# Kernel optimization log

Hardware: AMD Instinct MI355X
Metric: run time of the kernel (lower is better)

## Reference

```python
import jax, jax.numpy as jnp
import numpy as np

ALPHA = 0.25
GAMMA = 2.0
HUBER_DELTA = 0.5  # init kwarg delta
REG_BETA = 1.0 / 9.0


def calc_iou(a, b):
    # a: [A,4] anchors, b: [M,4] gt boxes, xyxy
    area = (b[:, 2] - b[:, 0]) * (b[:, 3] - b[:, 1])  # [M]
    iw = jnp.clip(jnp.minimum(a[:, 2:3], b[:, 2]) - jnp.maximum(a[:, 0:1], b[:, 0]), 0.0)
    ih = jnp.clip(jnp.minimum(a[:, 3:4], b[:, 3]) - jnp.maximum(a[:, 1:2], b[:, 1]), 0.0)
    ua = jnp.clip(((a[:, 2] - a[:, 0]) * (a[:, 3] - a[:, 1]))[:, None] + area - iw * ih, 1e-8)
    return iw * ih / ua  # [A,M]


def _per_sample(cls, reg, dist, ann, anchor):
    # cls [A,C], reg [A,4], dist [A,1], ann [M,6], anchor [A,4]
    aw = anchor[:, 2] - anchor[:, 0]
    ah = anchor[:, 3] - anchor[:, 1]
    acx = anchor[:, 0] + 0.5 * aw
    acy = anchor[:, 1] + 0.5 * ah

    valid = ann[:, 4] != -1.0  # padding annotations have class == -1
    cls = jnp.clip(cls, 1e-4, 1.0 - 1e-4)

    iou = jnp.where(valid[None, :], calc_iou(anchor, ann[:, :4]), -1.0)  # [A,M]
    iou_max = iou.max(axis=1)
    iou_arg = iou.argmax(axis=1)
    assigned = ann[iou_arg]  # [A,6]

    pos = iou_max >= 0.5
    num_pos = pos.sum()
    denom = jnp.maximum(num_pos.astype(cls.dtype), 1.0)

    labels = assigned[:, 4].astype(jnp.int32)
    onehot = jax.nn.one_hot(labels, cls.shape[1], dtype=cls.dtype)
    # -1 = ignore, 0 = negative (IoU<0.4 or positive-but-not-this-class), 1 = assigned class
    targets = jnp.where(pos[:, None], onehot,
                        jnp.where((iou_max < 0.4)[:, None], 0.0, -1.0))

    af = jnp.where(targets == 1.0, ALPHA, 1.0 - ALPHA)
    fw = af * jnp.where(targets == 1.0, 1.0 - cls, cls) ** GAMMA
    bce = -(targets * jnp.log(cls) + (1.0 - targets) * jnp.log(1.0 - cls))
    cls_loss = jnp.where(targets != -1.0, fw * bce, 0.0).sum() / denom

    # empty-annotation fallback: all anchors treated as background
    cls_loss_empty = ((1.0 - ALPHA) * cls ** GAMMA * (-jnp.log(1.0 - cls))).sum()
    has_ann = valid.any()
    cls_loss = jnp.where(has_ann, cls_loss, cls_loss_empty)

    gw_raw = assigned[:, 2] - assigned[:, 0]
    gh_raw = assigned[:, 3] - assigned[:, 1]
    gcx = assigned[:, 0] + 0.5 * gw_raw  # centers use unclamped w/h (as in torch code)
    gcy = assigned[:, 1] + 0.5 * gh_raw
    gw = jnp.clip(gw_raw, 1.0)
    gh = jnp.clip(gh_raw, 1.0)
    t = jnp.stack([(gcx - acx) / aw, (gcy - acy) / ah,
                   jnp.log(gw / aw), jnp.log(gh / ah)], axis=1)
    t = t / jnp.asarray([0.1, 0.1, 0.2, 0.2], dtype=cls.dtype)
    diff = jnp.abs(t - reg)
    rl = jnp.where(diff <= REG_BETA, 0.5 * 9.0 * diff ** 2, diff - 0.5 / 9.0)
    posf = pos.astype(cls.dtype)
    reg_loss = jnp.where(num_pos > 0, (rl * posf[:, None]).sum() / (denom * 4.0), 0.0)

    # --- distance Huber loss (delta=0.5), positives only ---
    d = jnp.abs(dist[:, 0] - assigned[:, 5])
    hl = jnp.where(d <= HUBER_DELTA, 0.5 * d ** 2, HUBER_DELTA * (d - 0.5 * HUBER_DELTA))
    dist_loss = jnp.where(num_pos > 0, (hl * posf).sum() / denom, 0.0)

    return cls_loss, reg_loss, dist_loss


def reference(classifications, regressions, distances, anchors, annotations):
    anchor = anchors[0]
    cl, rl, dl = jax.vmap(_per_sample, in_axes=(0, 0, 0, 0, None))(
        classifications, regressions, distances, annotations, anchor)
    return (jnp.mean(cl, keepdims=True),
            jnp.mean(rl, keepdims=True),
            jnp.mean(dl, keepdims=True))


def setup_inputs() -> dict:
    key = jax.random.key(0)
    ks = jax.random.split(key, 10)
    B, A, C, M = 8, 120000, 80, 32
    IMG = 800.0

    classifications = jax.random.uniform(ks[0], (B, A, C), dtype=jnp.float32)
    regressions = jax.random.normal(ks[1], (B, A, 4), dtype=jnp.float32)
    distances = jax.random.normal(ks[2], (B, A, 1), dtype=jnp.float32) * 10.0 + 50.0

    # anchors: valid xyxy boxes over an 800px image
    acx = jax.random.uniform(ks[3], (A,), minval=0.0, maxval=IMG)
    acy = jax.random.uniform(ks[4], (A,), minval=0.0, maxval=IMG)
    aw = jax.random.uniform(ks[5], (A, 2), minval=16.0, maxval=256.0)
    anchors = jnp.stack([acx - 0.5 * aw[:, 0], acy - 0.5 * aw[:, 1],
                         acx + 0.5 * aw[:, 0], acy + 0.5 * aw[:, 1]], axis=1)[None].astype(jnp.float32)

    # annotations: [B,M,6] = x1,y1,x2,y2,class,distance (all valid)
    gc = jax.random.uniform(ks[6], (B, M, 2), minval=100.0, maxval=IMG - 100.0)
    gs = jax.random.uniform(ks[7], (B, M, 2), minval=32.0, maxval=300.0)
    boxes = jnp.concatenate([gc - 0.5 * gs, gc + 0.5 * gs], axis=-1)
    labels = jax.random.randint(ks[8], (B, M, 1), 0, C).astype(jnp.float32)
    gdist = jax.random.uniform(ks[9], (B, M, 1), minval=1.0, maxval=100.0)
    annotations = jnp.concatenate([boxes, labels, gdist], axis=-1).astype(jnp.float32)

    return {"classifications": classifications, "regressions": regressions,
            "distances": distances, "anchors": anchors, "annotations": annotations}
```

## Files before the change

kernel.cpp:

```cpp
#include <hip/hip_runtime.h>
#include <hip/hip_bf16.h>


__device__ __forceinline__ float wave_reduce_sum(float v) {
#pragma unroll
    for (int off = 32; off > 0; off >>= 1) v += __shfl_down(v, off);
    return v;
}

__device__ __forceinline__ float smooth_l1(float d) {
    return d <= (1.0f / 9.0f) ? 4.5f * d * d : d - (0.5f / 9.0f);
}

template <int CPA>
__global__ __launch_bounds__(256) void fused_kernel(
    const float* __restrict__ cls, const float* __restrict__ reg,
    const float* __restrict__ dist, const float* __restrict__ anchors,
    const float* __restrict__ ann, float4* __restrict__ partials,
    int A, int M, int nb) {
    const int b = blockIdx.y;
    const int base = blockIdx.x << 8;
    const int tid = threadIdx.x;

    __shared__ float s_ann[64 * 6];
    __shared__ signed char s_state[256];
    const float* annb = ann + (size_t)b * M * 6;
    for (int i = tid; i < M * 6; i += 256) s_ann[i] = annb[i];
    s_state[tid] = -2;
    __syncthreads();

    const int a = base + tid;
    float l_npos = 0.f, l_reg = 0.f, l_dist = 0.f;
    if (a < A) {
        const float4 av = *(const float4*)(anchors + (size_t)a * 4);
        const float aw = av.z - av.x, ah = av.w - av.y;
        const float acx = av.x + 0.5f * aw, acy = av.y + 0.5f * ah;
        const float aarea = aw * ah;

        float best = -1.0f;
        int bi = 0;
        for (int m = 0; m < M; ++m) {
            const float* g = s_ann + m * 6;
            float iou = -1.0f;
            if (g[4] != -1.0f) {
                float iw = fmaxf(fminf(av.z, g[2]) - fmaxf(av.x, g[0]), 0.f);
                float ih = fmaxf(fminf(av.w, g[3]) - fmaxf(av.y, g[1]), 0.f);
                float inter = iw * ih;
                float area = (g[2] - g[0]) * (g[3] - g[1]);
                float ua = fmaxf(aarea + area - inter, 1e-8f);
                iou = inter / ua;
            }
            if (iou > best) { best = iou; bi = m; }
        }

        signed char st;
        if (best >= 0.5f) {
            const float* g = s_ann + bi * 6;
            st = (signed char)(int)g[4];
            l_npos = 1.f;
            const float4 rv = *(const float4*)(reg + ((size_t)b * A + a) * 4);
            const float gwr = g[2] - g[0], ghr = g[3] - g[1];
            const float gcx = g[0] + 0.5f * gwr, gcy = g[1] + 0.5f * ghr;
            const float gw = fmaxf(gwr, 1.f), gh = fmaxf(ghr, 1.f);
            const float t0 = ((gcx - acx) / aw) / 0.1f;
            const float t1 = ((gcy - acy) / ah) / 0.1f;
            const float t2 = __logf(gw / aw) / 0.2f;
            const float t3 = __logf(gh / ah) / 0.2f;
            l_reg = smooth_l1(fabsf(t0 - rv.x)) + smooth_l1(fabsf(t1 - rv.y)) +
                    smooth_l1(fabsf(t2 - rv.z)) + smooth_l1(fabsf(t3 - rv.w));
            const float dv = dist[(size_t)b * A + a];
            const float dd = fabsf(dv - g[5]);
            l_dist = dd <= 0.5f ? 0.5f * dd * dd : 0.5f * (dd - 0.25f);
        } else if (best < 0.4f) {
            st = -1;
        } else {
            st = -2;
        }
        s_state[tid] = st;
    }
    __syncthreads();

    const float4* __restrict__ clsb =
        (const float4*)(cls + ((size_t)b * A + base) * (CPA * 4));
    int a_local = tid / CPA;
    int cc = tid % CPA;
    constexpr int dA = 256 / CPA;
    constexpr int dC = 256 % CPA;
    float lsum = 0.f;
#pragma unroll 4
    for (int k = 0; k < CPA; ++k) {
        const int st = s_state[a_local];
        if (st != -2) {
            const float4 cv = clsb[k * 256 + tid];
            const int c0 = cc << 2;
#pragma unroll
            for (int j = 0; j < 4; ++j) {
                float c = j == 0 ? cv.x : j == 1 ? cv.y : j == 2 ? cv.z : cv.w;
                c = fminf(fmaxf(c, 1e-4f), 1.0f - 1e-4f);
                const bool ispos = (st == c0 + j);
                const float om = 1.0f - c;
                const float x = ispos ? c : om;
                const float w = ispos ? 0.25f * om * om : 0.75f * c * c;
                lsum -= w * __logf(x);
            }
        }
        a_local += dA;
        cc += dC;
        if (cc >= CPA) { cc -= CPA; ++a_local; }
    }

    __shared__ float s_red[4][4];
    const float w0 = wave_reduce_sum(l_npos);
    const float w1 = wave_reduce_sum(lsum);
    const float w2 = wave_reduce_sum(l_reg);
    const float w3 = wave_reduce_sum(l_dist);
    const int lane = tid & 63, wid = tid >> 6;
    if (lane == 0) {
        s_red[0][wid] = w0; s_red[1][wid] = w1; s_red[2][wid] = w2; s_red[3][wid] = w3;
    }
    __syncthreads();
    if (tid == 0) {
        float4 p;
        p.x = s_red[0][0] + s_red[0][1] + s_red[0][2] + s_red[0][3];
        p.y = s_red[1][0] + s_red[1][1] + s_red[1][2] + s_red[1][3];
        p.z = s_red[2][0] + s_red[2][1] + s_red[2][2] + s_red[2][3];
        p.w = s_red[3][0] + s_red[3][1] + s_red[3][2] + s_red[3][3];
        partials[(size_t)b * nb + blockIdx.x] = p;
    }
}

__global__ void finalize_kernel(const float4* __restrict__ partials,
                                float* __restrict__ out, int B, int nb) {
    const int lane = threadIdx.x & 63;
    const int b = threadIdx.x >> 6;
    __shared__ float s_res[8][3];
    if (b < B) {
        float np_ = 0.f, cs = 0.f, rs = 0.f, ds = 0.f;
        for (int i = lane; i < nb; i += 64) {
            const float4 p = partials[(size_t)b * nb + i];
            np_ += p.x; cs += p.y; rs += p.z; ds += p.w;
        }
        np_ = wave_reduce_sum(np_);
        cs = wave_reduce_sum(cs);
        rs = wave_reduce_sum(rs);
        ds = wave_reduce_sum(ds);
        if (lane == 0) {
            const float denom = fmaxf(np_, 1.f);
            s_res[b][0] = cs / denom;
            s_res[b][1] = np_ > 0.f ? rs / (denom * 4.f) : 0.f;
            s_res[b][2] = np_ > 0.f ? ds / denom : 0.f;
        }
    }
    __syncthreads();
    if (threadIdx.x == 0) {
        float c = 0.f, r = 0.f, d = 0.f;
        for (int i = 0; i < B; ++i) { c += s_res[i][0]; r += s_res[i][1]; d += s_res[i][2]; }
        out[0] = c / (float)B;
        out[1] = r / (float)B;
        out[2] = d / (float)B;
    }
}

__global__ __launch_bounds__(256) void fused_generic_kernel(
    const float* __restrict__ cls, const float* __restrict__ reg,
    const float* __restrict__ dist, const float* __restrict__ anchors,
    const float* __restrict__ ann, float4* __restrict__ partials,
    int A, int C, int M, int nb) {
    const int b = blockIdx.y;
    const int base = blockIdx.x << 8;
    const int tid = threadIdx.x;
    const int cpa = C >> 2;

    __shared__ float s_ann[64 * 6];
    __shared__ signed char s_state[256];
    const float* annb = ann + (size_t)b * M * 6;
    for (int i = tid; i < M * 6; i += 256) s_ann[i] = annb[i];
    s_state[tid] = -2;
    __syncthreads();

    const int a = base + tid;
    float l_npos = 0.f, l_reg = 0.f, l_dist = 0.f;
    if (a < A) {
        const float4 av = *(const float4*)(anchors + (size_t)a * 4);
        const float aw = av.z - av.x, ah = av.w - av.y;
        const float acx = av.x + 0.5f * aw, acy = av.y + 0.5f * ah;
        const float aarea = aw * ah;
        float best = -1.0f;
        int bi = 0;
        for (int m = 0; m < M; ++m) {
            const float* g = s_ann + m * 6;
            float iou = -1.0f;
            if (g[4] != -1.0f) {
                float iw = fmaxf(fminf(av.z, g[2]) - fmaxf(av.x, g[0]), 0.f);
                float ih = fmaxf(fminf(av.w, g[3]) - fmaxf(av.y, g[1]), 0.f);
                float inter = iw * ih;
                float area = (g[2] - g[0]) * (g[3] - g[1]);
                float ua = fmaxf(aarea + area - inter, 1e-8f);
                iou = inter / ua;
            }
            if (iou > best) { best = iou; bi = m; }
        }
        signed char st;
        if (best >= 0.5f) {
            const float* g = s_ann + bi * 6;
            st = (signed char)(int)g[4];
            l_npos = 1.f;
            const float4 rv = *(const float4*)(reg + ((size_t)b * A + a) * 4);
            const float gwr = g[2] - g[0], ghr = g[3] - g[1];
            const float gcx = g[0] + 0.5f * gwr, gcy = g[1] + 0.5f * ghr;
            const float gw = fmaxf(gwr, 1.f), gh = fmaxf(ghr, 1.f);
            const float t0 = ((gcx - acx) / aw) / 0.1f;
            const float t1 = ((gcy - acy) / ah) / 0.1f;
            const float t2 = __logf(gw / aw) / 0.2f;
            const float t3 = __logf(gh / ah) / 0.2f;
            l_reg = smooth_l1(fabsf(t0 - rv.x)) + smooth_l1(fabsf(t1 - rv.y)) +
                    smooth_l1(fabsf(t2 - rv.z)) + smooth_l1(fabsf(t3 - rv.w));
            const float dv = dist[(size_t)b * A + a];
            const float dd = fabsf(dv - g[5]);
            l_dist = dd <= 0.5f ? 0.5f * dd * dd : 0.5f * (dd - 0.25f);
        } else if (best < 0.4f) {
            st = -1;
        } else {
            st = -2;
        }
        s_state[tid] = st;
    }
    __syncthreads();

    const float4* __restrict__ clsb = (const float4*)(cls + ((size_t)b * A + base) * C);
    int a_local = tid / cpa;
    int cc = tid % cpa;
    const int dA = 256 / cpa;
    const int dC = 256 % cpa;
    float lsum = 0.f;
    for (int k = 0; k < cpa; ++k) {
        const int st = s_state[a_local];
        if (st != -2) {
            const float4 cv = clsb[k * 256 + tid];
            const int c0 = cc << 2;
#pragma unroll
            for (int j = 0; j < 4; ++j) {
                float c = j == 0 ? cv.x : j == 1 ? cv.y : j == 2 ? cv.z : cv.w;
                c = fminf(fmaxf(c, 1e-4f), 1.0f - 1e-4f);
                const bool ispos = (st == c0 + j);
                const float om = 1.0f - c;
                const float x = ispos ? c : om;
                const float w = ispos ? 0.25f * om * om : 0.75f * c * c;
                lsum -= w * __logf(x);
            }
        }
        a_local += dA;
        cc += dC;
        if (cc >= cpa) { cc -= cpa; ++a_local; }
    }

    __shared__ float s_red[4][4];
    const float w0 = wave_reduce_sum(l_npos);
    const float w1 = wave_reduce_sum(lsum);
    const float w2 = wave_reduce_sum(l_reg);
    const float w3 = wave_reduce_sum(l_dist);
    const int lane = tid & 63, wid = tid >> 6;
    if (lane == 0) {
        s_red[0][wid] = w0; s_red[1][wid] = w1; s_red[2][wid] = w2; s_red[3][wid] = w3;
    }
    __syncthreads();
    if (tid == 0) {
        float4 p;
        p.x = s_red[0][0] + s_red[0][1] + s_red[0][2] + s_red[0][3];
        p.y = s_red[1][0] + s_red[1][1] + s_red[1][2] + s_red[1][3];
        p.z = s_red[2][0] + s_red[2][1] + s_red[2][2] + s_red[2][3];
        p.w = s_red[3][0] + s_red[3][1] + s_red[3][2] + s_red[3][3];
        partials[(size_t)b * nb + blockIdx.x] = p;
    }
}

extern "C" void kernel_launch(void* const* d_in, const int* in_sizes, int n_in,
                              void* d_out, int out_size, void* d_ws, size_t ws_size,
                              hipStream_t stream) {
    const float* cls     = (const float*)d_in[0];
    const float* reg     = (const float*)d_in[1];
    const float* dist    = (const float*)d_in[2];
    const float* anchors = (const float*)d_in[3];
    const float* ann     = (const float*)d_in[4];

    const int A = in_sizes[3] / 4;
    const int B = in_sizes[1] / (A * 4);
    const int C = in_sizes[0] / (B * A);
    const int M = in_sizes[4] / (B * 6);
    const int nb = (A + 255) / 256;

    float4* partials = (float4*)d_ws;

    dim3 g(nb, B), blk(256);
    if (C == 80) {
        fused_kernel<20><<<g, blk, 0, stream>>>(cls, reg, dist, anchors, ann,
                                                partials, A, M, nb);
    } else {
        fused_generic_kernel<<<g, blk, 0, stream>>>(cls, reg, dist, anchors, ann,
                                                    partials, A, C, M, nb);
    }
    finalize_kernel<<<1, B * 64, 0, stream>>>(partials, (float*)d_out, B, nb);
}
```

Baseline: 92.20 us.

## Compute background focal loss unconditionally and apply sparse per-anchor corrections

The classification loop now sums the negative focal term for every class of every anchor without first waiting on the IoU assignment, using nontemporal loads issued before the IoU loop. Ignored anchors and the positive class entry are then corrected sparsely: a wave ballot walks the non-background anchors, subtracting the full row for ignored anchors and swapping in the positive term for the assigned class. This removes the shared-memory state array and the barrier between assignment and the streaming loop, so the bulk class loads can overlap the IoU work. In exchange it adds serial per-anchor wave loops whose cost grows with the number of positive and ignored anchors, and it changes floating-point summation order.

```diff
diff --git a/kernel.cpp b/kernel.cpp
--- a/kernel.cpp
+++ b/kernel.cpp
@@ -1,6 +1,10 @@
 #include <hip/hip_runtime.h>
 #include <hip/hip_bf16.h>
 
+
+typedef float v4f __attribute__((ext_vector_type(4)));
+
+#define LN2_075 0.51986038542f
 
 __device__ __forceinline__ float wave_reduce_sum(float v) {
 #pragma unroll
@@ -21,16 +25,44 @@
     const int b = blockIdx.y;
     const int base = blockIdx.x << 8;
     const int tid = threadIdx.x;
+    const int lane = tid & 63;
 
     __shared__ float s_ann[64 * 6];
-    __shared__ signed char s_state[256];
     const float* annb = ann + (size_t)b * M * 6;
     for (int i = tid; i < M * 6; i += 256) s_ann[i] = annb[i];
-    s_state[tid] = -2;
+
+    const v4f* __restrict__ clsb = (const v4f*)(cls + ((size_t)b * A + base) * (CPA * 4));
+    float acc2 = 0.f;
+    if (base + 256 <= A) {
+#pragma unroll
+        for (int k = 0; k < CPA; ++k) {
+            const v4f cv = __builtin_nontemporal_load(&clsb[k * 256 + tid]);
+#pragma unroll
+            for (int j = 0; j < 4; ++j) {
+                const float c = fminf(fmaxf(cv[j], 1e-4f), 1.0f - 1e-4f);
+                acc2 = fmaf(c * c, __log2f(1.0f - c), acc2);
+            }
+        }
+    } else {
+        const int nch = (A - base) * CPA;
+        for (int k = 0; k < CPA; ++k) {
+            const int idx = k * 256 + tid;
+            if (idx < nch) {
+                const v4f cv = __builtin_nontemporal_load(&clsb[idx]);
+#pragma unroll
+                for (int j = 0; j < 4; ++j) {
+                    const float c = fminf(fmaxf(cv[j], 1e-4f), 1.0f - 1e-4f);
+                    acc2 = fmaf(c * c, __log2f(1.0f - c), acc2);
+                }
+            }
+        }
+    }
+
     __syncthreads();
 
     const int a = base + tid;
     float l_npos = 0.f, l_reg = 0.f, l_dist = 0.f;
+    int st = -1;
     if (a < A) {
         const float4 av = *(const float4*)(anchors + (size_t)a * 4);
         const float aw = av.z - av.x, ah = av.w - av.y;
@@ -53,6 +85,150 @@
             if (iou > best) { best = iou; bi = m; }
         }
 
+        if (best >= 0.5f) {
+            const float* g = s_ann + bi * 6;
+            st = (int)g[4];
+            l_npos = 1.f;
+            const float4 rv = *(const float4*)(reg + ((size_t)b * A + a) * 4);
+            const float gwr = g[2] - g[0], ghr = g[3] - g[1];
+            const float gcx = g[0] + 0.5f * gwr, gcy = g[1] + 0.5f * ghr;
+            const float gw = fmaxf(gwr, 1.f), gh = fmaxf(ghr, 1.f);
+            const float t0 = ((gcx - acx) / aw) / 0.1f;
+            const float t1 = ((gcy - acy) / ah) / 0.1f;
+            const float t2 = __logf(gw / aw) / 0.2f;
+            const float t3 = __logf(gh / ah) / 0.2f;
+            l_reg = smooth_l1(fabsf(t0 - rv.x)) + smooth_l1(fabsf(t1 - rv.y)) +
+                    smooth_l1(fabsf(t2 - rv.z)) + smooth_l1(fabsf(t3 - rv.w));
+            const float dv = dist[(size_t)b * A + a];
+            const float dd = fabsf(dv - g[5]);
+            l_dist = dd <= 0.5f ? 0.5f * dd * dd : 0.5f * (dd - 0.25f);
+        } else if (best >= 0.4f) {
+            st = -2;
+        }
+    }
+
+    float corr = 0.f;
+    unsigned long long mask = __ballot(st != -1);
+    const int wbase = tid & ~63;
+    while (mask) {
+        const int bit = (int)__ffsll(mask) - 1;
+        mask &= mask - 1;
+        const int sst = __shfl(st, bit);
+        const int la = wbase + bit;
+        if (sst == -2) {
+            float part = 0.f;
+            if (lane < CPA) {
+                const v4f cv = clsb[(size_t)la * CPA + lane];
+#pragma unroll
+                for (int j = 0; j < 4; ++j) {
+                    const float c = fminf(fmaxf(cv[j], 1e-4f), 1.0f - 1e-4f);
+                    part = fmaf(c * c, __log2f(1.0f - c), part);
+                }
+            }
+            part = wave_reduce_sum(part);
+            if (lane == 0) corr += LN2_075 * part;
+        } else if (lane == 0) {
+            const float cr = cls[((size_t)b * A + base + la) * (CPA * 4) + sst];
+            const float c = fminf(fmaxf(cr, 1e-4f), 1.0f - 1e-4f);
+            const float om = 1.0f - c;
+            corr += LN2_075 * (c * c * __log2f(om))
+                    + 0.25f * om * om * (-__logf(c));
+        }
+    }
+
+    const float lsum = fmaf(acc2, -LN2_075, corr);
+
+    __shared__ float s_red[4][4];
+    const float w0 = wave_reduce_sum(l_npos);
+    const float w1 = wave_reduce_sum(lsum);
+    const float w2 = wave_reduce_sum(l_reg);
+    const float w3 = wave_reduce_sum(l_dist);
+    const int wid = tid >> 6;
+    if (lane == 0) {
+        s_red[0][wid] = w0; s_red[1][wid] = w1; s_red[2][wid] = w2; s_red[3][wid] = w3;
+    }
+    __syncthreads();
+    if (tid == 0) {
+        float4 p;
+        p.x = s_red[0][0] + s_red[0][1] + s_red[0][2] + s_red[0][3];
+        p.y = s_red[1][0] + s_red[1][1] + s_red[1][2] + s_red[1][3];
+        p.z = s_red[2][0] + s_red[2][1] + s_red[2][2] + s_red[2][3];
+        p.w = s_red[3][0] + s_red[3][1] + s_red[3][2] + s_red[3][3];
+        partials[(size_t)b * nb + blockIdx.x] = p;
+    }
+}
+
+__global__ void finalize_kernel(const float4* __restrict__ partials,
+                                float* __restrict__ out, int B, int nb) {
+    const int lane = threadIdx.x & 63;
+    const int b = threadIdx.x >> 6;
+    __shared__ float s_res[8][3];
+    if (b < B) {
+        float np_ = 0.f, cs = 0.f, rs = 0.f, ds = 0.f;
+        for (int i = lane; i < nb; i += 64) {
+            const float4 p = partials[(size_t)b * nb + i];
+            np_ += p.x; cs += p.y; rs += p.z; ds += p.w;
+        }
+        np_ = wave_reduce_sum(np_);
+        cs = wave_reduce_sum(cs);
+        rs = wave_reduce_sum(rs);
+        ds = wave_reduce_sum(ds);
+        if (lane == 0) {
+            const float denom = fmaxf(np_, 1.f);
+            s_res[b][0] = cs / denom;
+            s_res[b][1] = np_ > 0.f ? rs / (denom * 4.f) : 0.f;
+            s_res[b][2] = np_ > 0.f ? ds / denom : 0.f;
+        }
+    }
+    __syncthreads();
+    if (threadIdx.x == 0) {
+        float c = 0.f, r = 0.f, d = 0.f;
+        for (int i = 0; i < B; ++i) { c += s_res[i][0]; r += s_res[i][1]; d += s_res[i][2]; }
+        out[0] = c / (float)B;
+        out[1] = r / (float)B;
+        out[2] = d / (float)B;
+    }
+}
+
+__global__ __launch_bounds__(256) void fused_generic_kernel(
+    const float* __restrict__ cls, const float* __restrict__ reg,
+    const float* __restrict__ dist, const float* __restrict__ anchors,
+    const float* __restrict__ ann, float4* __restrict__ partials,
+    int A, int C, int M, int nb) {
+    const int b = blockIdx.y;
+    const int base = blockIdx.x << 8;
+    const int tid = threadIdx.x;
+    const int cpa = C >> 2;
+
+    __shared__ float s_ann[64 * 6];
+    __shared__ signed char s_state[256];
+    const float* annb = ann + (size_t)b * M * 6;
+    for (int i = tid; i < M * 6; i += 256) s_ann[i] = annb[i];
+    s_state[tid] = -2;
+    __syncthreads();
+
+    const int a = base + tid;
+    float l_npos = 0.f, l_reg = 0.f, l_dist = 0.f;
+    if (a < A) {
+        const float4 av = *(const float4*)(anchors + (size_t)a * 4);
+        const float aw = av.z - av.x, ah = av.w - av.y;
+        const float acx = av.x + 0.5f * aw, acy = av.y + 0.5f * ah;
+        const float aarea = aw * ah;
+        float best = -1.0f;
+        int bi = 0;
+        for (int m = 0; m < M; ++m) {
+            const float* g = s_ann + m * 6;
+            float iou = -1.0f;
+            if (g[4] != -1.0f) {
+                float iw = fmaxf(fminf(av.z, g[2]) - fmaxf(av.x, g[0]), 0.f);
+                float ih = fmaxf(fminf(av.w, g[3]) - fmaxf(av.y, g[1]), 0.f);
+                float inter = iw * ih;
+                float area = (g[2] - g[0]) * (g[3] - g[1]);
+                float ua = fmaxf(aarea + area - inter, 1e-8f);
+                iou = inter / ua;
+            }
+            if (iou > best) { best = iou; bi = m; }
+        }
         signed char st;
         if (best >= 0.5f) {
             const float* g = s_ann + bi * 6;
@@ -80,153 +256,6 @@
     }
     __syncthreads();
 
-    const float4* __restrict__ clsb =
-        (const float4*)(cls + ((size_t)b * A + base) * (CPA * 4));
-    int a_local = tid / CPA;
-    int cc = tid % CPA;
-    constexpr int dA = 256 / CPA;
-    constexpr int dC = 256 % CPA;
-    float lsum = 0.f;
-#pragma unroll 4
-    for (int k = 0; k < CPA; ++k) {
-        const int st = s_state[a_local];
-        if (st != -2) {
-            const float4 cv = clsb[k * 256 + tid];
-            const int c0 = cc << 2;
-#pragma unroll
-            for (int j = 0; j < 4; ++j) {
-                float c = j == 0 ? cv.x : j == 1 ? cv.y : j == 2 ? cv.z : cv.w;
-                c = fminf(fmaxf(c, 1e-4f), 1.0f - 1e-4f);
-                const bool ispos = (st == c0 + j);
-                const float om = 1.0f - c;
-                const float x = ispos ? c : om;
-                const float w = ispos ? 0.25f * om * om : 0.75f * c * c;
-                lsum -= w * __logf(x);
-            }
-        }
-        a_local += dA;
-        cc += dC;
-        if (cc >= CPA) { cc -= CPA; ++a_local; }
-    }
-
-    __shared__ float s_red[4][4];
-    const float w0 = wave_reduce_sum(l_npos);
-    const float w1 = wave_reduce_sum(lsum);
-    const float w2 = wave_reduce_sum(l_reg);
-    const float w3 = wave_reduce_sum(l_dist);
-    const int lane = tid & 63, wid = tid >> 6;
-    if (lane == 0) {
-        s_red[0][wid] = w0; s_red[1][wid] = w1; s_red[2][wid] = w2; s_red[3][wid] = w3;
-    }
-    __syncthreads();
-    if (tid == 0) {
-        float4 p;
-        p.x = s_red[0][0] + s_red[0][1] + s_red[0][2] + s_red[0][3];
-        p.y = s_red[1][0] + s_red[1][1] + s_red[1][2] + s_red[1][3];
-        p.z = s_red[2][0] + s_red[2][1] + s_red[2][2] + s_red[2][3];
-        p.w = s_red[3][0] + s_red[3][1] + s_red[3][2] + s_red[3][3];
-        partials[(size_t)b * nb + blockIdx.x] = p;
-    }
-}
-
-__global__ void finalize_kernel(const float4* __restrict__ partials,
-                                float* __restrict__ out, int B, int nb) {
-    const int lane = threadIdx.x & 63;
-    const int b = threadIdx.x >> 6;
-    __shared__ float s_res[8][3];
-    if (b < B) {
-        float np_ = 0.f, cs = 0.f, rs = 0.f, ds = 0.f;
-        for (int i = lane; i < nb; i += 64) {
-            const float4 p = partials[(size_t)b * nb + i];
-            np_ += p.x; cs += p.y; rs += p.z; ds += p.w;
-        }
-        np_ = wave_reduce_sum(np_);
-        cs = wave_reduce_sum(cs);
-        rs = wave_reduce_sum(rs);
-        ds = wave_reduce_sum(ds);
-        if (lane == 0) {
-            const float denom = fmaxf(np_, 1.f);
-            s_res[b][0] = cs / denom;
-            s_res[b][1] = np_ > 0.f ? rs / (denom * 4.f) : 0.f;
-            s_res[b][2] = np_ > 0.f ? ds / denom : 0.f;
-        }
-    }
-    __syncthreads();
-    if (threadIdx.x == 0) {
-        float c = 0.f, r = 0.f, d = 0.f;
-        for (int i = 0; i < B; ++i) { c += s_res[i][0]; r += s_res[i][1]; d += s_res[i][2]; }
-        out[0] = c / (float)B;
-        out[1] = r / (float)B;
-        out[2] = d / (float)B;
-    }
-}
-
-__global__ __launch_bounds__(256) void fused_generic_kernel(
-    const float* __restrict__ cls, const float* __restrict__ reg,
-    const float* __restrict__ dist, const float* __restrict__ anchors,
-    const float* __restrict__ ann, float4* __restrict__ partials,
-    int A, int C, int M, int nb) {
-    const int b = blockIdx.y;
-    const int base = blockIdx.x << 8;
-    const int tid = threadIdx.x;
-    const int cpa = C >> 2;
-
-    __shared__ float s_ann[64 * 6];
-    __shared__ signed char s_state[256];
-    const float* annb = ann + (size_t)b * M * 6;
-    for (int i = tid; i < M * 6; i += 256) s_ann[i] = annb[i];
-    s_state[tid] = -2;
-    __syncthreads();
-
-    const int a = base + tid;
-    float l_npos = 0.f, l_reg = 0.f, l_dist = 0.f;
-    if (a < A) {
-        const float4 av = *(const float4*)(anchors + (size_t)a * 4);
-        const float aw = av.z - av.x, ah = av.w - av.y;
-        const float acx = av.x + 0.5f * aw, acy = av.y + 0.5f * ah;
-        const float aarea = aw * ah;
-        float best = -1.0f;
-        int bi = 0;
-        for (int m = 0; m < M; ++m) {
-            const float* g = s_ann + m * 6;
-            float iou = -1.0f;
-            if (g[4] != -1.0f) {
-                float iw = fmaxf(fminf(av.z, g[2]) - fmaxf(av.x, g[0]), 0.f);
-                float ih = fmaxf(fminf(av.w, g[3]) - fmaxf(av.y, g[1]), 0.f);
-                float inter = iw * ih;
-                float area = (g[2] - g[0]) * (g[3] - g[1]);
-                float ua = fmaxf(aarea + area - inter, 1e-8f);
-                iou = inter / ua;
-            }
-            if (iou > best) { best = iou; bi = m; }
-        }
-        signed char st;
-        if (best >= 0.5f) {
-            const float* g = s_ann + bi * 6;
-            st = (signed char)(int)g[4];
-            l_npos = 1.f;
-            const float4 rv = *(const float4*)(reg + ((size_t)b * A + a) * 4);
-            const float gwr = g[2] - g[0], ghr = g[3] - g[1];
-            const float gcx = g[0] + 0.5f * gwr, gcy = g[1] + 0.5f * ghr;
-            const float gw = fmaxf(gwr, 1.f), gh = fmaxf(ghr, 1.f);
-            const float t0 = ((gcx - acx) / aw) / 0.1f;
-            const float t1 = ((gcy - acy) / ah) / 0.1f;
-            const float t2 = __logf(gw / aw) / 0.2f;
-            const float t3 = __logf(gh / ah) / 0.2f;
-            l_reg = smooth_l1(fabsf(t0 - rv.x)) + smooth_l1(fabsf(t1 - rv.y)) +
-                    smooth_l1(fabsf(t2 - rv.z)) + smooth_l1(fabsf(t3 - rv.w));
-            const float dv = dist[(size_t)b * A + a];
-            const float dd = fabsf(dv - g[5]);
-            l_dist = dd <= 0.5f ? 0.5f * dd * dd : 0.5f * (dd - 0.25f);
-        } else if (best < 0.4f) {
-            st = -1;
-        } else {
-            st = -2;
-        }
-        s_state[tid] = st;
-    }
-    __syncthreads();
-
     const float4* __restrict__ clsb = (const float4*)(cls + ((size_t)b * A + base) * C);
     int a_local = tid / cpa;
     int cc = tid % cpa;
```

After: 84.13 us. -8.8%, faster.
